# Kernel optimization log

Hardware: AMD Instinct MI355X
Metric: run time of the kernel (lower is better)

Reference implementation:

```python
import jax, jax.numpy as jnp
import numpy as np

N_NODES = 100000
N_EDGES = 1600000
D_FEAT = 64
UNITS = [128, 128]


def setup_inputs() -> dict:
    key = jax.random.key(0)
    ks = jax.random.split(key, 8)
    row = jax.random.randint(ks[0], (N_EDGES,), 0, N_NODES, dtype=jnp.int32)
    col = jax.random.randint(ks[1], (N_EDGES,), 0, N_NODES, dtype=jnp.int32)
    vals = jax.random.uniform(ks[2], (N_EDGES,), dtype=jnp.float32)
    H = jax.random.normal(ks[3], (N_NODES, D_FEAT), dtype=jnp.float32)
    W1 = jax.random.normal(ks[4], (D_FEAT, UNITS[0]), dtype=jnp.float32) * (1.0 / np.sqrt(D_FEAT))
    b1 = jnp.zeros((UNITS[0],), dtype=jnp.float32)
    W2 = jax.random.normal(ks[5], (UNITS[0], UNITS[1]), dtype=jnp.float32) * (1.0 / np.sqrt(UNITS[0]))
    b2 = jnp.zeros((UNITS[1],), dtype=jnp.float32)
    return {"row": row, "col": col, "vals": vals, "H": H,
            "W1": W1, "b1": b1, "W2": W2, "b2": b2}


def _spmm(row, col, vals, H, n_nodes):
    # sparse A (COO) @ dense H: gather source rows, scale, scatter-add to dest
    return jax.ops.segment_sum(vals[:, None] * H[col], row, num_segments=n_nodes)


def reference(row, col, vals, H, W1, b1, W2, b2):
    n = H.shape[0]
    # layer 0: AH @ W1 + b1, relu (source bug: relu applied since i < num_units-1)
    AH = _spmm(row, col, vals, H, n)
    H1 = jax.nn.relu(AH @ W1 + b1)
    # layer 1: same structure, also relu per source's activation condition
    AH1 = _spmm(row, col, vals, H1, n)
    H2 = jax.nn.relu(AH1 @ W2 + b2)
    return H2
```

## Files before the change

kernel.cpp:

```cpp
#include <hip/hip_runtime.h>


#define NFEAT 64
#define NHID 128
#define BSHIFT 9
#define BROWS (1 << BSHIFT)
#define NB_MAX 256

typedef __attribute__((ext_vector_type(8))) short bf16x8;
typedef __attribute__((ext_vector_type(4))) float f32x4;
typedef __attribute__((ext_vector_type(2))) float f32x2;

__device__ __forceinline__ unsigned short f2bf(float x) {
  unsigned u = __float_as_uint(x);
  unsigned r = (u + 0x7FFFu + ((u >> 16) & 1u)) >> 16;
  return (unsigned short)r;
}
__device__ __forceinline__ unsigned pack2(float a, float b) {
  return (unsigned)f2bf(a) | ((unsigned)f2bf(b) << 16);
}

__device__ __forceinline__ unsigned pk_fp8x4(float a, float b, float c, float d) {
  int w = __builtin_amdgcn_cvt_pk_fp8_f32(a, b, 0, false);
  w = __builtin_amdgcn_cvt_pk_fp8_f32(c, d, w, true);
  return (unsigned)w;
}
__device__ __forceinline__ unsigned char f2fp8(float x) {
  return (unsigned char)(__builtin_amdgcn_cvt_pk_fp8_f32(x, 0.f, 0, false) & 0xFF);
}

__device__ __forceinline__ void acc16(f32x2* a, uint4 q, float v) {
  f32x2 vv = {v, v};
  a[0] += vv * __builtin_amdgcn_cvt_pk_f32_fp8(q.x, false);
  a[1] += vv * __builtin_amdgcn_cvt_pk_f32_fp8(q.x, true);
  a[2] += vv * __builtin_amdgcn_cvt_pk_f32_fp8(q.y, false);
  a[3] += vv * __builtin_amdgcn_cvt_pk_f32_fp8(q.y, true);
  a[4] += vv * __builtin_amdgcn_cvt_pk_f32_fp8(q.z, false);
  a[5] += vv * __builtin_amdgcn_cvt_pk_f32_fp8(q.z, true);
  a[6] += vv * __builtin_amdgcn_cvt_pk_f32_fp8(q.w, false);
  a[7] += vv * __builtin_amdgcn_cvt_pk_f32_fp8(q.w, true);
}

template <int RS>
__device__ __forceinline__ void gather_row(
    const int2* __restrict__ sedge, const uint4* __restrict__ Hq,
    int beg, int end, int f, f32x2* a) {
  int j = beg;
  if ((j & 1) && j < end) {
    int2 ev = sedge[j];
    acc16(a, Hq[ev.x * RS + f], __int_as_float(ev.y));
    ++j;
  }
  for (; j + 4 <= end; j += 4) {
    int4 p0 = ((const int4*)sedge)[j >> 1];
    int4 p1 = ((const int4*)sedge)[(j >> 1) + 1];
    uint4 q0 = Hq[p0.x * RS + f];
    uint4 q1 = Hq[p0.z * RS + f];
    uint4 q2 = Hq[p1.x * RS + f];
    uint4 q3 = Hq[p1.z * RS + f];
    acc16(a, q0, __int_as_float(p0.y));
    acc16(a, q1, __int_as_float(p0.w));
    acc16(a, q2, __int_as_float(p1.y));
    acc16(a, q3, __int_as_float(p1.w));
  }
  for (; j < end; ++j) {
    int2 ev = sedge[j];
    acc16(a, Hq[ev.x * RS + f], __int_as_float(ev.y));
  }
}

__global__ __launch_bounds__(256) void prep_kernel(
    const float* __restrict__ H, const float* __restrict__ W1,
    const float* __restrict__ W2, unsigned char* __restrict__ Hf8,
    unsigned short* __restrict__ Wsw1, unsigned short* __restrict__ Wsw2,
    int n8) {
  const int total = n8 + 64 * 128 + 128 * 128;
  for (int w = blockIdx.x * 256 + threadIdx.x; w < total; w += gridDim.x * 256) {
    if (w < n8) {
      float4 a = ((const float4*)H)[2 * w];
      float4 b = ((const float4*)H)[2 * w + 1];
      ((uint2*)Hf8)[w] = make_uint2(pk_fp8x4(a.x, a.y, a.z, a.w),
                                    pk_fp8x4(b.x, b.y, b.z, b.w));
    } else {
      int idx = w - n8;
      const float* W = W1;
      unsigned short* Wsw = Wsw1;
      if (idx >= 64 * 128) {
        idx -= 64 * 128;
        W = W2;
        Wsw = Wsw2;
      }
      int j = idx & 7, q = (idx >> 3) & 3, nn = (idx >> 5) & 127, kt = idx >> 12;
      int k = kt * 32 + q * 8 + j;
      Wsw[idx] = f2bf(W[(size_t)k * 128 + nn]);
    }
  }
}

__global__ __launch_bounds__(256) void bhist_kernel(
    const int* __restrict__ row, int* __restrict__ bcnt, int n_edges, int nb) {
  __shared__ int h[NB_MAX];
  for (int i = threadIdx.x; i < NB_MAX; i += 256) h[i] = 0;
  __syncthreads();
  const int n4 = n_edges >> 2;
  for (int i = blockIdx.x * 256 + threadIdx.x; i < n4; i += gridDim.x * 256) {
    int4 r4 = ((const int4*)row)[i];
    atomicAdd(&h[r4.x >> BSHIFT], 1);
    atomicAdd(&h[r4.y >> BSHIFT], 1);
    atomicAdd(&h[r4.z >> BSHIFT], 1);
    atomicAdd(&h[r4.w >> BSHIFT], 1);
  }
  if (blockIdx.x == 0 && threadIdx.x < (n_edges & 3))
    atomicAdd(&h[row[(n4 << 2) + threadIdx.x] >> BSHIFT], 1);
  __syncthreads();
  for (int i = threadIdx.x; i < nb; i += 256)
    if (h[i]) atomicAdd(&bcnt[i], h[i]);
}

__global__ __launch_bounds__(NB_MAX) void bscan_kernel(
    const int* __restrict__ bcnt, int* __restrict__ bbase, int* __restrict__ cur,
    int* __restrict__ row_ptr, int nb, int n) {
  __shared__ int sm[NB_MAX];
  int t = threadIdx.x;
  int v = (t < nb) ? bcnt[t] : 0;
  sm[t] = v;
  __syncthreads();
  for (int off = 1; off < NB_MAX; off <<= 1) {
    int u = (t >= off) ? sm[t - off] : 0;
    __syncthreads();
    sm[t] += u;
    __syncthreads();
  }
  if (t < nb) {
    bbase[t] = sm[t] - v;
    cur[t] = sm[t] - v;
  }
  if (t == nb - 1) {
    bbase[nb] = sm[t];
    row_ptr[n] = sm[t];
  }
}

__global__ __launch_bounds__(1024) void partition_kernel(
    const int* __restrict__ row, const int* __restrict__ col,
    const float* __restrict__ vals, int* __restrict__ cur,
    int2* __restrict__ bedge, int n_edges) {
  __shared__ int h[NB_MAX], base[NB_MAX], rk[NB_MAX];
  for (int i = threadIdx.x; i < NB_MAX; i += 1024) {
    h[i] = 0;
    rk[i] = 0;
  }
  __syncthreads();
  const int start = blockIdx.x * 1024 + threadIdx.x;
  const int step = gridDim.x * 1024;
  for (int e = start; e < n_edges; e += step)
    atomicAdd(&h[row[e] >> BSHIFT], 1);
  __syncthreads();
  for (int i = threadIdx.x; i < NB_MAX; i += 1024)
    base[i] = h[i] ? atomicAdd(&cur[i], h[i]) : 0;
  __syncthreads();
  for (int e = start; e < n_edges; e += step) {
    int r = row[e];
    int b = r >> BSHIFT;
    int rl = r & (BROWS - 1);
    int p = base[b] + atomicAdd(&rk[b], 1);
    bedge[p] = make_int2((rl << 17) | col[e], __float_as_int(vals[e]));
  }
}

__global__ __launch_bounds__(1024) void bucket_csr_kernel(
    const int* __restrict__ bbase, const int2* __restrict__ bedge,
    int* __restrict__ row_ptr, int2* __restrict__ sedge, int n) {
  __shared__ int cnt[BROWS];
  __shared__ int sm[BROWS];
  const int b = blockIdx.x;
  const int t = threadIdx.x;
  const int beg = bbase[b], end = bbase[b + 1];
  if (t < BROWS) cnt[t] = 0;
  __syncthreads();
  for (int j = beg + t; j < end; j += 1024)
    atomicAdd(&cnt[((unsigned)bedge[j].x) >> 17], 1);
  __syncthreads();
  int v = (t < BROWS) ? cnt[t] : 0;
  if (t < BROWS) sm[t] = v;
  __syncthreads();
  for (int off = 1; off < BROWS; off <<= 1) {
    int u = (t >= off && t < BROWS) ? sm[t - off] : 0;
    __syncthreads();
    if (t < BROWS) sm[t] += u;
    __syncthreads();
  }
  int incl = (t < BROWS) ? sm[t] : 0;
  __syncthreads();
  if (t < BROWS) {
    sm[t] = incl - v;
    int r = (b << BSHIFT) + t;
    if (r < n) row_ptr[r] = beg + sm[t];
    cnt[t] = 0;
  }
  __syncthreads();
  for (int j = beg + t; j < end; j += 1024) {
    int2 ev = bedge[j];
    int rl = ((unsigned)ev.x) >> 17;
    int rank = atomicAdd(&cnt[rl], 1);
    sedge[beg + sm[rl] + rank] = make_int2(ev.x & 0x1FFFF, ev.y);
  }
}

__global__ __launch_bounds__(256) void fused64_kernel(
    const int* __restrict__ row_ptr, const int2* __restrict__ sedge,
    const unsigned char* __restrict__ Hf8,
    const unsigned short* __restrict__ Wsw,
    const float* __restrict__ b, unsigned char* __restrict__ H1f8, int n) {
  __shared__ uint4 tile[64 * 9];
  const int tid = threadIdx.x;
  {
    const int rl = tid >> 2, f = tid & 3;
    const int r = blockIdx.x * 64 + rl;
    int beg = 0, end = 0;
    if (r < n) {
      beg = row_ptr[r];
      end = row_ptr[r + 1];
    }
    f32x2 a[8];
#pragma unroll
    for (int i = 0; i < 8; ++i) a[i] = (f32x2){0.f, 0.f};
    gather_row<4>(sedge, (const uint4*)Hf8, beg, end, f, a);
    tile[rl * 9 + f * 2] =
        make_uint4(pack2(a[0].x, a[0].y), pack2(a[1].x, a[1].y),
                   pack2(a[2].x, a[2].y), pack2(a[3].x, a[3].y));
    tile[rl * 9 + f * 2 + 1] =
        make_uint4(pack2(a[4].x, a[4].y), pack2(a[5].x, a[5].y),
                   pack2(a[6].x, a[6].y), pack2(a[7].x, a[7].y));
  }
  const int lane = tid & 63, wave = tid >> 6;
  const int m = lane & 15, quad = lane >> 4;
  bf16x8 bfr[2][8];
#pragma unroll
  for (int kt = 0; kt < 2; ++kt)
#pragma unroll
    for (int c = 0; c < 8; ++c)
      bfr[kt][c] = *(const bf16x8*)(Wsw + ((size_t)(kt * 128 + c * 16 + m)) * 32 + quad * 8);
  __syncthreads();
  f32x4 acc[8];
#pragma unroll
  for (int c = 0; c < 8; ++c) acc[c] = (f32x4){0.f, 0.f, 0.f, 0.f};
#pragma unroll
  for (int kt = 0; kt < 2; ++kt) {
    bf16x8 a = *(const bf16x8*)&tile[(wave * 16 + m) * 9 + kt * 4 + quad];
#pragma unroll
    for (int c = 0; c < 8; ++c)
      acc[c] = __builtin_amdgcn_mfma_f32_16x16x32_bf16(a, bfr[kt][c], acc[c], 0, 0, 0);
  }
  const int r0 = blockIdx.x * 64 + wave * 16;
#pragma unroll
  for (int c = 0; c < 8; ++c) {
    float bias = b[c * 16 + m];
#pragma unroll
    for (int i = 0; i < 4; ++i) {
      int rr = r0 + quad * 4 + i;
      if (rr >= n) continue;
      H1f8[(size_t)rr * 128 + c * 16 + m] = f2fp8(fmaxf(acc[c][i] + bias, 0.f));
    }
  }
}

__global__ __launch_bounds__(512) void fused128_kernel(
    const int* __restrict__ row_ptr, const int2* __restrict__ sedge,
    const unsigned char* __restrict__ H1f8,
    const unsigned short* __restrict__ Wsw,
    const float* __restrict__ b, float* __restrict__ out, int n) {
  __shared__ uint4 tile[64 * 17];
  const int tid = threadIdx.x;
  {
    const int rl = tid >> 3, f = tid & 7;
    const int r = blockIdx.x * 64 + rl;
    int beg = 0, end = 0;
    if (r < n) {
      beg = row_ptr[r];
      end = row_ptr[r + 1];
    }
    f32x2 a[8];
#pragma unroll
    for (int i = 0; i < 8; ++i) a[i] = (f32x2){0.f, 0.f};
    gather_row<8>(sedge, (const uint4*)H1f8, beg, end, f, a);
    tile[rl * 17 + f * 2] =
        make_uint4(pack2(a[0].x, a[0].y), pack2(a[1].x, a[1].y),
                   pack2(a[2].x, a[2].y), pack2(a[3].x, a[3].y));
    tile[rl * 17 + f * 2 + 1] =
        make_uint4(pack2(a[4].x, a[4].y), pack2(a[5].x, a[5].y),
                   pack2(a[6].x, a[6].y), pack2(a[7].x, a[7].y));
  }
  const int lane = tid & 63, wave = tid >> 6;
  const int m = lane & 15, quad = lane >> 4;
  const int g = wave >> 1, h = wave & 1;
  bf16x8 bfr[4][4];
#pragma unroll
  for (int kt = 0; kt < 4; ++kt)
#pragma unroll
    for (int c = 0; c < 4; ++c)
      bfr[kt][c] = *(const bf16x8*)(Wsw + ((size_t)(kt * 128 + (h * 4 + c) * 16 + m)) * 32 + quad * 8);
  __syncthreads();
  f32x4 acc[4];
#pragma unroll
  for (int c = 0; c < 4; ++c) acc[c] = (f32x4){0.f, 0.f, 0.f, 0.f};
#pragma unroll
  for (int kt = 0; kt < 4; ++kt) {
    bf16x8 a = *(const bf16x8*)&tile[(g * 16 + m) * 17 + kt * 4 + quad];
#pragma unroll
    for (int c = 0; c < 4; ++c)
      acc[c] = __builtin_amdgcn_mfma_f32_16x16x32_bf16(a, bfr[kt][c], acc[c], 0, 0, 0);
  }
  const int r0 = blockIdx.x * 64 + g * 16;
#pragma unroll
  for (int c = 0; c < 4; ++c) {
    float bias = b[(h * 4 + c) * 16 + m];
#pragma unroll
    for (int i = 0; i < 4; ++i) {
      int rr = r0 + quad * 4 + i;
      if (rr >= n) continue;
      out[(size_t)rr * 128 + (h * 4 + c) * 16 + m] = fmaxf(acc[c][i] + bias, 0.f);
    }
  }
}

__global__ __launch_bounds__(256) void spmm64_atomic(
    const int* __restrict__ row, const int* __restrict__ col,
    const float* __restrict__ vals, const float* __restrict__ Hin,
    float* __restrict__ out, int n_edges) {
  int tid = blockIdx.x * 256 + threadIdx.x;
  int e = tid >> 4, f = tid & 15;
  if (e >= n_edges) return;
  int c = col[e], r = row[e];
  float v = vals[e];
  float4 h = ((const float4*)Hin)[(size_t)c * 16 + f];
  float* o = out + (size_t)r * 64 + f * 4;
  atomicAdd(o + 0, v * h.x);
  atomicAdd(o + 1, v * h.y);
  atomicAdd(o + 2, v * h.z);
  atomicAdd(o + 3, v * h.w);
}

__global__ __launch_bounds__(256) void spmm128_atomic(
    const int* __restrict__ row, const int* __restrict__ col,
    const float* __restrict__ vals, const float* __restrict__ Hin,
    float* __restrict__ out, int n_edges) {
  int tid = blockIdx.x * 256 + threadIdx.x;
  int e = tid >> 5, f = tid & 31;
  if (e >= n_edges) return;
  int c = col[e], r = row[e];
  float v = vals[e];
  float4 h = ((const float4*)Hin)[(size_t)c * 32 + f];
  float* o = out + (size_t)r * 128 + f * 4;
  atomicAdd(o + 0, v * h.x);
  atomicAdd(o + 1, v * h.y);
  atomicAdd(o + 2, v * h.z);
  atomicAdd(o + 3, v * h.w);
}

template <int K>
__global__ __launch_bounds__(256) void gemm_tiled_relu(
    const float* __restrict__ A, const float* __restrict__ W,
    const float* __restrict__ b, float* __restrict__ out, int n) {
  constexpr int KB = 32;
  constexpr int RP = 132;
  __shared__ float As[KB][RP];
  __shared__ float Ws[KB][128];
  const int t = threadIdx.x;
  const int tx = t & 15, ty = t >> 4;
  const int r0 = blockIdx.x * 128;
  float4 acc0[8], acc1[8];
#pragma unroll
  for (int i = 0; i < 8; ++i) {
    acc0[i] = make_float4(0.f, 0.f, 0.f, 0.f);
    acc1[i] = make_float4(0.f, 0.f, 0.f, 0.f);
  }
  for (int k0 = 0; k0 < K; k0 += KB) {
#pragma unroll
    for (int q = 0; q < 4; ++q) {
      int f = q * 256 + t;
      int kk = f >> 5, cv = f & 31;
      ((float4*)&Ws[kk][0])[cv] = ((const float4*)(W + (size_t)(k0 + kk) * 128))[cv];
    }
#pragma unroll
    for (int q = 0; q < 4; ++q) {
      int f = q * 256 + t;
      int r = f >> 3, kv = f & 7;
      float4 av = make_float4(0.f, 0.f, 0.f, 0.f);
      if (r0 + r < n) av = ((const float4*)(A + (size_t)(r0 + r) * K + k0))[kv];
      As[4 * kv + 0][r] = av.x;
      As[4 * kv + 1][r] = av.y;
      As[4 * kv + 2][r] = av.z;
      As[4 * kv + 3][r] = av.w;
    }
    __syncthreads();
#pragma unroll
    for (int k = 0; k < KB; ++k) {
      float4 w0 = *((const float4*)&Ws[k][4 * tx]);
      float4 w1 = *((const float4*)&Ws[k][64 + 4 * tx]);
#pragma unroll
      for (int i = 0; i < 8; ++i) {
        float a = As[k][ty + 16 * i];
        acc0[i].x = fmaf(a, w0.x, acc0[i].x);
        acc0[i].y = fmaf(a, w0.y, acc0[i].y);
        acc0[i].z = fmaf(a, w0.z, acc0[i].z);
        acc0[i].w = fmaf(a, w0.w, acc0[i].w);
        acc1[i].x = fmaf(a, w1.x, acc1[i].x);
        acc1[i].y = fmaf(a, w1.y, acc1[i].y);
        acc1[i].z = fmaf(a, w1.z, acc1[i].z);
        acc1[i].w = fmaf(a, w1.w, acc1[i].w);
      }
    }
    __syncthreads();
  }
  float4 bb0 = ((const float4*)b)[tx];
  float4 bb1 = ((const float4*)(b + 64))[tx];
#pragma unroll
  for (int i = 0; i < 8; ++i) {
    int r = r0 + ty + 16 * i;
    if (r >= n) continue;
    float4 o0, o1;
    o0.x = fmaxf(acc0[i].x + bb0.x, 0.f);
    o0.y = fmaxf(acc0[i].y + bb0.y, 0.f);
    o0.z = fmaxf(acc0[i].z + bb0.z, 0.f);
    o0.w = fmaxf(acc0[i].w + bb0.w, 0.f);
    o1.x = fmaxf(acc1[i].x + bb1.x, 0.f);
    o1.y = fmaxf(acc1[i].y + bb1.y, 0.f);
    o1.z = fmaxf(acc1[i].z + bb1.z, 0.f);
    o1.w = fmaxf(acc1[i].w + bb1.w, 0.f);
    ((float4*)(out + (size_t)r * 128))[tx] = o0;
    ((float4*)(out + (size_t)r * 128 + 64))[tx] = o1;
  }
}

extern "C" void kernel_launch(void* const* d_in, const int* in_sizes, int n_in,
                              void* d_out, int out_size, void* d_ws, size_t ws_size,
                              hipStream_t stream) {
  const int* row = (const int*)d_in[0];
  const int* col = (const int*)d_in[1];
  const float* vals = (const float*)d_in[2];
  const float* H = (const float*)d_in[3];
  const float* W1 = (const float*)d_in[4];
  const float* b1 = (const float*)d_in[5];
  const float* W2 = (const float*)d_in[6];
  const float* b2 = (const float*)d_in[7];
  float* out = (float*)d_out;

  const int n_edges = in_sizes[0];
  const int n_nodes = in_sizes[3] / NFEAT;
  const int nb = (n_nodes + BROWS - 1) / BROWS;
  const int fused_grid = (n_nodes + 63) / 64;

  size_t off = 0;
  char* base = (char*)d_ws;
  int2* bedge = (int2*)(base + off);  off += (size_t)n_edges * 8;
  unsigned char* Hf8 = (unsigned char*)(base + off);   off += (size_t)n_nodes * NFEAT;
  unsigned char* H1f8 = (unsigned char*)(base + off);  off += (size_t)n_nodes * NHID;
  int2* sedge = (int2*)(base + off);  off += (size_t)n_edges * 8;
  unsigned short* Wsw1 = (unsigned short*)(base + off); off += 64 * 128 * 2;
  unsigned short* Wsw2 = (unsigned short*)(base + off); off += 128 * 128 * 2;
  int* bcnt = (int*)(base + off);     off += NB_MAX * 4;
  int* bbase = (int*)(base + off);    off += (NB_MAX + 1) * 4;
  int* cur = (int*)(base + off);      off += NB_MAX * 4;
  int* row_ptr = (int*)(base + off);  off += ((size_t)n_nodes + 1) * 4;
  const size_t needed = off;

  if (ws_size >= needed && nb <= NB_MAX && n_nodes <= (1 << 17)) {
    hipMemsetAsync(bcnt, 0, NB_MAX * sizeof(int), stream);
    bhist_kernel<<<1024, 256, 0, stream>>>(row, bcnt, n_edges, nb);
    bscan_kernel<<<1, NB_MAX, 0, stream>>>(bcnt, bbase, cur, row_ptr, nb, n_nodes);
    partition_kernel<<<256, 1024, 0, stream>>>(row, col, vals, cur, bedge, n_edges);
    bucket_csr_kernel<<<nb, 1024, 0, stream>>>(bbase, bedge, row_ptr, sedge, n_nodes);

    prep_kernel<<<1024, 256, 0, stream>>>(H, W1, W2, Hf8, Wsw1, Wsw2,
                                          n_nodes * NFEAT / 8);

    fused64_kernel<<<fused_grid, 256, 0, stream>>>(
        row_ptr, sedge, Hf8, Wsw1, b1, H1f8, n_nodes);
    fused128_kernel<<<fused_grid, 512, 0, stream>>>(
        row_ptr, sedge, H1f8, Wsw2, b2, out, n_nodes);
  } else {
    float* fAH = (float*)d_ws;
    float* fH1 = fAH + (size_t)n_nodes * NFEAT;
    hipMemsetAsync(fAH, 0, (size_t)n_nodes * NFEAT * sizeof(float), stream);
    hipMemsetAsync(out, 0, (size_t)n_nodes * NHID * sizeof(float), stream);
    spmm64_atomic<<<(n_edges * 16 + 255) / 256, 256, 0, stream>>>(row, col, vals, H, fAH, n_edges);
    gemm_tiled_relu<64><<<(n_nodes + 127) / 128, 256, 0, stream>>>(fAH, W1, b1, fH1, n_nodes);
    spmm128_atomic<<<(n_edges * 32 + 255) / 256, 256, 0, stream>>>(row, col, vals, fH1, out, n_edges);
    gemm_tiled_relu<128><<<(n_nodes + 127) / 128, 256, 0, stream>>>(out, W2, b2, out, n_nodes);
  }
}
```

Measured before the change: 271.7 us.

## Prefetch edge metadata in gather, vectorize partition reads, shrink fused128 blocks

New measurement: 264.4 us. -2.7%, faster.

```diff
diff --git a/kernel.cpp b/kernel.cpp
--- a/kernel.cpp
+++ b/kernel.cpp
@@ -51,17 +51,33 @@
     acc16(a, Hq[ev.x * RS + f], __int_as_float(ev.y));
     ++j;
   }
-  for (; j + 4 <= end; j += 4) {
-    int4 p0 = ((const int4*)sedge)[j >> 1];
-    int4 p1 = ((const int4*)sedge)[(j >> 1) + 1];
-    uint4 q0 = Hq[p0.x * RS + f];
-    uint4 q1 = Hq[p0.z * RS + f];
-    uint4 q2 = Hq[p1.x * RS + f];
-    uint4 q3 = Hq[p1.z * RS + f];
-    acc16(a, q0, __int_as_float(p0.y));
-    acc16(a, q1, __int_as_float(p0.w));
-    acc16(a, q2, __int_as_float(p1.y));
-    acc16(a, q3, __int_as_float(p1.w));
+  if (j + 4 <= end) {
+    const int4* mp = (const int4*)sedge;
+    int4 m0 = mp[j >> 1], m1 = mp[(j >> 1) + 1];
+    while (j + 8 <= end) {
+      uint4 q0 = Hq[m0.x * RS + f];
+      uint4 q1 = Hq[m0.z * RS + f];
+      uint4 q2 = Hq[m1.x * RS + f];
+      uint4 q3 = Hq[m1.z * RS + f];
+      int4 n0 = mp[(j >> 1) + 2];
+      int4 n1 = mp[(j >> 1) + 3];
+      acc16(a, q0, __int_as_float(m0.y));
+      acc16(a, q1, __int_as_float(m0.w));
+      acc16(a, q2, __int_as_float(m1.y));
+      acc16(a, q3, __int_as_float(m1.w));
+      m0 = n0;
+      m1 = n1;
+      j += 4;
+    }
+    uint4 q0 = Hq[m0.x * RS + f];
+    uint4 q1 = Hq[m0.z * RS + f];
+    uint4 q2 = Hq[m1.x * RS + f];
+    uint4 q3 = Hq[m1.z * RS + f];
+    acc16(a, q0, __int_as_float(m0.y));
+    acc16(a, q1, __int_as_float(m0.w));
+    acc16(a, q2, __int_as_float(m1.y));
+    acc16(a, q3, __int_as_float(m1.w));
+    j += 4;
   }
   for (; j < end; ++j) {
     int2 ev = sedge[j];
@@ -151,20 +167,53 @@
     rk[i] = 0;
   }
   __syncthreads();
-  const int start = blockIdx.x * 1024 + threadIdx.x;
-  const int step = gridDim.x * 1024;
-  for (int e = start; e < n_edges; e += step)
-    atomicAdd(&h[row[e] >> BSHIFT], 1);
+  const int t0 = blockIdx.x * 1024 + threadIdx.x;
+  const int T = gridDim.x * 1024;
+  const int n4 = n_edges >> 2;
+  for (int i = t0; i < n4; i += T) {
+    int4 r4 = ((const int4*)row)[i];
+    atomicAdd(&h[r4.x >> BSHIFT], 1);
+    atomicAdd(&h[r4.y >> BSHIFT], 1);
+    atomicAdd(&h[r4.z >> BSHIFT], 1);
+    atomicAdd(&h[r4.w >> BSHIFT], 1);
+  }
+  if (blockIdx.x == 0 && threadIdx.x < (n_edges & 3))
+    atomicAdd(&h[row[(n4 << 2) + threadIdx.x] >> BSHIFT], 1);
   __syncthreads();
   for (int i = threadIdx.x; i < NB_MAX; i += 1024)
     base[i] = h[i] ? atomicAdd(&cur[i], h[i]) : 0;
   __syncthreads();
-  for (int e = start; e < n_edges; e += step) {
+  for (int i = t0; i < n4; i += T) {
+    int4 r4 = ((const int4*)row)[i];
+    int4 c4 = ((const int4*)col)[i];
+    float4 v4 = ((const float4*)vals)[i];
+    {
+      int b = r4.x >> BSHIFT;
+      int p = base[b] + atomicAdd(&rk[b], 1);
+      bedge[p] = make_int2(((r4.x & (BROWS - 1)) << 17) | c4.x, __float_as_int(v4.x));
+    }
+    {
+      int b = r4.y >> BSHIFT;
+      int p = base[b] + atomicAdd(&rk[b], 1);
+      bedge[p] = make_int2(((r4.y & (BROWS - 1)) << 17) | c4.y, __float_as_int(v4.y));
+    }
+    {
+      int b = r4.z >> BSHIFT;
+      int p = base[b] + atomicAdd(&rk[b], 1);
+      bedge[p] = make_int2(((r4.z & (BROWS - 1)) << 17) | c4.z, __float_as_int(v4.z));
+    }
+    {
+      int b = r4.w >> BSHIFT;
+      int p = base[b] + atomicAdd(&rk[b], 1);
+      bedge[p] = make_int2(((r4.w & (BROWS - 1)) << 17) | c4.w, __float_as_int(v4.w));
+    }
+  }
+  if (blockIdx.x == 0 && threadIdx.x < (n_edges & 3)) {
+    int e = (n4 << 2) + threadIdx.x;
     int r = row[e];
     int b = r >> BSHIFT;
-    int rl = r & (BROWS - 1);
     int p = base[b] + atomicAdd(&rk[b], 1);
-    bedge[p] = make_int2((rl << 17) | col[e], __float_as_int(vals[e]));
+    bedge[p] = make_int2(((r & (BROWS - 1)) << 17) | col[e], __float_as_int(vals[e]));
   }
 }
 
@@ -265,16 +314,16 @@
   }
 }
 
-__global__ __launch_bounds__(512) void fused128_kernel(
+__global__ __launch_bounds__(256) void fused128_kernel(
     const int* __restrict__ row_ptr, const int2* __restrict__ sedge,
     const unsigned char* __restrict__ H1f8,
     const unsigned short* __restrict__ Wsw,
     const float* __restrict__ b, float* __restrict__ out, int n) {
-  __shared__ uint4 tile[64 * 17];
+  __shared__ uint4 tile[32 * 17];
   const int tid = threadIdx.x;
   {
     const int rl = tid >> 3, f = tid & 7;
-    const int r = blockIdx.x * 64 + rl;
+    const int r = blockIdx.x * 32 + rl;
     int beg = 0, end = 0;
     if (r < n) {
       beg = row_ptr[r];
@@ -311,7 +360,7 @@
     for (int c = 0; c < 4; ++c)
       acc[c] = __builtin_amdgcn_mfma_f32_16x16x32_bf16(a, bfr[kt][c], acc[c], 0, 0, 0);
   }
-  const int r0 = blockIdx.x * 64 + g * 16;
+  const int r0 = blockIdx.x * 32 + g * 16;
 #pragma unroll
   for (int c = 0; c < 4; ++c) {
     float bias = b[(h * 4 + c) * 16 + m];
@@ -449,7 +498,6 @@
   const int n_edges = in_sizes[0];
   const int n_nodes = in_sizes[3] / NFEAT;
   const int nb = (n_nodes + BROWS - 1) / BROWS;
-  const int fused_grid = (n_nodes + 63) / 64;
 
   size_t off = 0;
   char* base = (char*)d_ws;
@@ -475,9 +523,9 @@
     prep_kernel<<<1024, 256, 0, stream>>>(H, W1, W2, Hf8, Wsw1, Wsw2,
                                           n_nodes * NFEAT / 8);
 
-    fused64_kernel<<<fused_grid, 256, 0, stream>>>(
+    fused64_kernel<<<(n_nodes + 63) / 64, 256, 0, stream>>>(
         row_ptr, sedge, Hf8, Wsw1, b1, H1f8, n_nodes);
-    fused128_kernel<<<fused_grid, 512, 0, stream>>>(
+    fused128_kernel<<<(n_nodes + 31) / 32, 256, 0, stream>>>(
         row_ptr, sedge, H1f8, Wsw2, b2, out, n_nodes);
   } else {
     float* fAH = (float*)d_ws;
```
